# Kernel tuning notes

Hardware: AMD Instinct MI355X
Metric: run time of the kernel (lower is better)

Reference implementation:

```python
import jax, jax.numpy as jnp
import numpy as np

B, D, L = 64, 1024, 2048  # batch, init dim, source length; context feature dim = D//2


def setup_inputs() -> dict:
    key = jax.random.key(0)
    k1, k2, k3, k4 = jax.random.split(key, 4)
    inp = jax.random.normal(k1, (B, D), dtype=jnp.float32)
    context = jax.random.normal(k2, (B, L, D // 2), dtype=jnp.float32)
    # torch Linear weights: [out_features, in_features]
    W_in = jax.random.normal(k3, (D, D), dtype=jnp.float32) * (1.0 / np.sqrt(D))
    W_out = jax.random.normal(k4, (D, 2 * D), dtype=jnp.float32) * (1.0 / np.sqrt(2 * D))
    return {"input": inp, "context": context, "W_in": W_in, "W_out": W_out}


def reference(input, context, W_in, W_out):
    Bv, Dv = input.shape
    # linear_in(input).view(B, D//2, 2): two query vectors of size D//2 per batch
    targetT = (input @ W_in.T).reshape(Bv, Dv // 2, 2)           # [B, D/2, 2]
    attn = jnp.einsum('bld,bdk->bkl', context, targetT)          # [B, 2, L]
    attn = jax.nn.softmax(attn, axis=-1)                         # softmax over sourceL
    weighted = jnp.einsum('bkl,bld->bkd', attn, context)         # [B, 2, D/2]
    weightedContext = weighted.reshape(Bv, Dv)                   # [B, D]
    combined = jnp.concatenate([weightedContext, input], axis=1) # [B, 2D]
    contextOutput = jnp.tanh(combined @ W_out.T)                 # [B, D]
    return contextOutput, attn[:, 0, :], attn[:, 1, :]
```

## Files before the change

### kernel.cpp

```cpp
#include <hip/hip_runtime.h>
#include <cmath>

#define NB 64
#define ND 1024
#define DH 512
#define NL 2048
#define NCHUNK 16
#define RPB 128
#define RPW 32
#define REC 520
#define KS 32

typedef float f4 __attribute__((ext_vector_type(4)));
__device__ __forceinline__ f4 ntld(const float* p) {
  return __builtin_nontemporal_load((const f4*)p);
}

template <int KK>
__global__ __launch_bounds__(256, 4) void k_gemm(const float* __restrict__ A,
                                                 const float* __restrict__ W,
                                                 float* __restrict__ part) {
  constexpr int SLAB = KK / KS;
  __shared__ float As[64][36];
  const int t = threadIdx.x;
  const int lane = t & 63;
  const int wv = t >> 6;
  const int k0 = blockIdx.y * SLAB;
  const int j0 = __builtin_amdgcn_readfirstlane((int)(blockIdx.x * 32 + wv * 8));
  const float* Wb = W + (size_t)j0 * KK + k0;

  float acc[8];
#pragma unroll
  for (int j = 0; j < 8; j++) acc[j] = 0.f;

  const int srow = t >> 2, sko = (t & 3) * 8;
  const float* sbase = A + (size_t)srow * KK + k0 + sko;

  for (int kc = 0; kc < SLAB; kc += 32) {
    float4 v0 = *(const float4*)(sbase + kc);
    float4 v1 = *(const float4*)(sbase + kc + 4);
    __syncthreads();
    *(float4*)&As[srow][sko]     = v0;
    *(float4*)&As[srow][sko + 4] = v1;
    __syncthreads();
#pragma unroll
    for (int kk = 0; kk < 32; kk += 4) {
      float4 av = *(const float4*)&As[lane][kk];
      const float* wp = Wb + kc + kk;
#pragma unroll
      for (int j = 0; j < 8; j++) {
        float4 wq = *(const float4*)(wp + (size_t)j * KK);
        acc[j] = fmaf(av.x, wq.x, acc[j]);
        acc[j] = fmaf(av.y, wq.y, acc[j]);
        acc[j] = fmaf(av.z, wq.z, acc[j]);
        acc[j] = fmaf(av.w, wq.w, acc[j]);
      }
    }
  }
  float* p = part + ((size_t)blockIdx.y * 64 + lane) * ND + j0;
  *(float4*)(p)     = make_float4(acc[0], acc[1], acc[2], acc[3]);
  *(float4*)(p + 4) = make_float4(acc[4], acc[5], acc[6], acc[7]);
}

template <int ACT>
__global__ __launch_bounds__(64) void k_reduce(const float* __restrict__ part,
                                               float* __restrict__ out) {
  const int i = (blockIdx.x * 64 + threadIdx.x) * 4;
  float4 s = make_float4(0.f, 0.f, 0.f, 0.f);
#pragma unroll 8
  for (int ks = 0; ks < KS; ks++) {
    f4 v = ntld(part + (size_t)ks * (64 * ND) + i);
    s.x += v.x; s.y += v.y; s.z += v.z; s.w += v.w;
  }
  if (ACT) { s.x = tanhf(s.x); s.y = tanhf(s.y); s.z = tanhf(s.z); s.w = tanhf(s.w); }
  *(float4*)(out + i) = s;
}

__global__ __launch_bounds__(256, 4) void k2_attn(const float* __restrict__ ctx,
                                                  const float* __restrict__ tgt,
                                                  float* __restrict__ sc0,
                                                  float* __restrict__ sc1,
                                                  float* __restrict__ part) {
  const int chunk = blockIdx.x, b = blockIdx.y;
  const int wave = threadIdx.x >> 6, lane = threadIdx.x & 63;
  const float* crow = ctx + ((size_t)b * NL + chunk * RPB + wave * RPW) * DH + lane * 8;

  float t0[8], t1[8];
  {
    const float* tp = tgt + b * ND + lane * 16;
#pragma unroll
    for (int j = 0; j < 4; j++) {
      float4 v = *(const float4*)(tp + j * 4);
      t0[2 * j] = v.x; t1[2 * j] = v.y; t0[2 * j + 1] = v.z; t1[2 * j + 1] = v.w;
    }
  }

  float m0 = -INFINITY, l0 = 0.f, m1 = -INFINITY, l1 = 0.f;
  float a0[8], a1[8];
#pragma unroll
  for (int j = 0; j < 8; j++) { a0[j] = 0.f; a1[j] = 0.f; }
  float sv0 = 0.f, sv1 = 0.f;

  f4 cur[4], nxt[4];
  cur[0] = ntld(crow);
  cur[1] = ntld(crow + 4);
  cur[2] = ntld(crow + DH);
  cur[3] = ntld(crow + DH + 4);

#pragma unroll 2
  for (int ib = 0; ib < 16; ib++) {
    if (ib < 15) {
      const float* p = crow + (size_t)(2 * ib + 2) * DH;
      nxt[0] = ntld(p);
      nxt[1] = ntld(p + 4);
      nxt[2] = ntld(p + DH);
      nxt[3] = ntld(p + DH + 4);
    }
    const float* C = (const float*)cur;

    float s0[2], s1[2];
#pragma unroll
    for (int r = 0; r < 2; r++) {
      float x0 = 0.f, x1 = 0.f;
#pragma unroll
      for (int j = 0; j < 8; j++) { x0 += C[r * 8 + j] * t0[j]; x1 += C[r * 8 + j] * t1[j]; }
      s0[r] = x0; s1[r] = x1;
    }
#pragma unroll
    for (int off = 32; off; off >>= 1) {
      s0[0] += __shfl_xor(s0[0], off);
      s0[1] += __shfl_xor(s0[1], off);
      s1[0] += __shfl_xor(s1[0], off);
      s1[1] += __shfl_xor(s1[1], off);
    }
#pragma unroll
    for (int r = 0; r < 2; r++)
      if (lane == 2 * ib + r) { sv0 = s0[r]; sv1 = s1[r]; }

    {
      float mn = fmaxf(m0, fmaxf(s0[0], s0[1]));
      float al = __expf(m0 - mn);
      float p0 = __expf(s0[0] - mn), p1 = __expf(s0[1] - mn);
      l0 = l0 * al + p0 + p1;
      m0 = mn;
#pragma unroll
      for (int j = 0; j < 8; j++)
        a0[j] = a0[j] * al + p0 * C[j] + p1 * C[8 + j];
    }
    {
      float mn = fmaxf(m1, fmaxf(s1[0], s1[1]));
      float al = __expf(m1 - mn);
      float p0 = __expf(s1[0] - mn), p1 = __expf(s1[1] - mn);
      l1 = l1 * al + p0 + p1;
      m1 = mn;
#pragma unroll
      for (int j = 0; j < 8; j++)
        a1[j] = a1[j] * al + p0 * C[j] + p1 * C[8 + j];
    }
#pragma unroll
    for (int i = 0; i < 4; i++) cur[i] = nxt[i];
  }

  const int rowbase = b * NL + chunk * RPB + wave * RPW;
  if (lane < RPW) { sc0[rowbase + lane] = sv0; sc1[rowbase + lane] = sv1; }

  __shared__ float accS[4][1024];
  __shared__ float mlS[4][4];
  *(float4*)&accS[wave][lane * 8]           = make_float4(a0[0], a0[1], a0[2], a0[3]);
  *(float4*)&accS[wave][lane * 8 + 4]       = make_float4(a0[4], a0[5], a0[6], a0[7]);
  *(float4*)&accS[wave][512 + lane * 8]     = make_float4(a1[0], a1[1], a1[2], a1[3]);
  *(float4*)&accS[wave][512 + lane * 8 + 4] = make_float4(a1[4], a1[5], a1[6], a1[7]);
  if (lane == 0) { mlS[wave][0] = m0; mlS[wave][1] = l0; mlS[wave][2] = m1; mlS[wave][3] = l1; }
  __syncthreads();

  const int t = threadIdx.x;
  const int k = (t * 4) >> 9;
  const int d = (t * 4) & 511;
  float M = fmaxf(fmaxf(mlS[0][2 * k], mlS[1][2 * k]), fmaxf(mlS[2][2 * k], mlS[3][2 * k]));
  float Lk = 0.f;
  float v0 = 0.f, v1 = 0.f, v2 = 0.f, v3 = 0.f;
#pragma unroll
  for (int w = 0; w < 4; w++) {
    float e = __expf(mlS[w][2 * k] - M);
    Lk += mlS[w][2 * k + 1] * e;
    const float* ap = &accS[w][k * 512 + d];
    v0 += ap[0] * e; v1 += ap[1] * e; v2 += ap[2] * e; v3 += ap[3] * e;
  }
  float* rec = part + ((size_t)(b * NCHUNK + chunk) * 2 + k) * REC;
  if ((t & 127) == 0) { rec[0] = M; rec[1] = Lk; }
  *(float4*)&rec[4 + d] = make_float4(v0, v1, v2, v3);
}

__global__ __launch_bounds__(256) void k3_combine(const float* __restrict__ part,
                                                  const float* __restrict__ inp,
                                                  float* __restrict__ combined,
                                                  float* __restrict__ sc0,
                                                  float* __restrict__ sc1) {
  const int b = blockIdx.x >> 2, q = blockIdx.x & 3;
  const int t = threadIdx.x;
  __shared__ float MM[2], LL[2];
  __shared__ float eS[2][NCHUNK];
  if (t < 2) {
    const int k = t;
    float Mk = -INFINITY;
#pragma unroll
    for (int c = 0; c < NCHUNK; c++)
      Mk = fmaxf(Mk, part[((size_t)(b * NCHUNK + c) * 2 + k) * REC]);
    float Lk = 0.f;
#pragma unroll
    for (int c = 0; c < NCHUNK; c++) {
      const float* rec = part + ((size_t)(b * NCHUNK + c) * 2 + k) * REC;
      Lk += rec[1] * __expf(rec[0] - Mk);
    }
    MM[k] = Mk; LL[k] = Lk;
  }
  __syncthreads();
  if (t < 2 * NCHUNK) {
    const int k = t >> 4, c = t & 15;
    eS[k][c] = __expf(part[((size_t)(b * NCHUNK + c) * 2 + k) * REC] - MM[k]);
  }
  __syncthreads();

  const int k = t >> 7, d = q * 128 + (t & 127);
  float v = 0.f;
#pragma unroll
  for (int c = 0; c < NCHUNK; c++)
    v += part[((size_t)(b * NCHUNK + c) * 2 + k) * REC + 4 + d] * eS[k][c];
  combined[(size_t)b * 2048 + k * 512 + d] = v / LL[k];

  combined[(size_t)b * 2048 + 1024 + q * 256 + t] = inp[(size_t)b * ND + q * 256 + t];

  const float M0 = MM[0], i0 = 1.f / LL[0];
  const float M1 = MM[1], i1 = 1.f / LL[1];
  const int pos = b * NL + q * 512 + t * 2;
  float2 x0 = *(const float2*)(sc0 + pos);
  float2 x1 = *(const float2*)(sc1 + pos);
  x0.x = __expf(x0.x - M0) * i0; x0.y = __expf(x0.y - M0) * i0;
  x1.x = __expf(x1.x - M1) * i1; x1.y = __expf(x1.y - M1) * i1;
  *(float2*)(sc0 + pos) = x0;
  *(float2*)(sc1 + pos) = x1;
}

extern "C" void kernel_launch(void* const* d_in, const int* in_sizes, int n_in,
                              void* d_out, int out_size, void* d_ws, size_t ws_size,
                              hipStream_t stream) {
  const float* input   = (const float*)d_in[0];
  const float* context = (const float*)d_in[1];
  const float* W_in    = (const float*)d_in[2];
  const float* W_out   = (const float*)d_in[3];

  float* out   = (float*)d_out;
  float* attn0 = out + NB * ND;
  float* attn1 = attn0 + NB * NL;

  float* ws       = (float*)d_ws;
  float* target   = ws;
  float* combined = target + NB * ND;
  float* apart    = combined + NB * 2048;
  float* gpart    = apart + NB * NCHUNK * 2 * REC;

  k_gemm<ND><<<dim3(32, KS), dim3(256), 0, stream>>>(input, W_in, gpart);
  k_reduce<0><<<dim3(256), dim3(64), 0, stream>>>(gpart, target);
  k2_attn<<<dim3(NCHUNK, NB), dim3(256), 0, stream>>>(context, target, attn0, attn1, apart);
  k3_combine<<<dim3(4 * NB), dim3(256), 0, stream>>>(apart, input, combined, attn0, attn1);
  k_gemm<2 * ND><<<dim3(32, KS), dim3(256), 0, stream>>>(combined, W_out, gpart);
  k_reduce<1><<<dim3(256), dim3(64), 0, stream>>>(gpart, out);
}
```

Before: 391.9 us.

## Fuse combine and final reduce into producers via last-block atomic counters

Drops the separate combine and final reduce launches. The last attention block to finish for each batch row, and the last k-slab block for each output column tile of the second GEMM, now does the cross-block merge. Completion is detected with agent-scope atomic counters that are reset in the first reduce kernel. This removes two kernel launches and their gaps. In exchange the final merge runs on only a few blocks, which serialises that tail work, and the change adds threadfence and atomic overhead.

```diff
diff --git a/kernel.cpp b/kernel.cpp
--- a/kernel.cpp
+++ b/kernel.cpp
@@ -16,10 +16,12 @@
   return __builtin_nontemporal_load((const f4*)p);
 }
 
-template <int KK>
+template <int KK, int FUSE>
 __global__ __launch_bounds__(256, 4) void k_gemm(const float* __restrict__ A,
                                                  const float* __restrict__ W,
-                                                 float* __restrict__ part) {
+                                                 float* __restrict__ part,
+                                                 float* __restrict__ out,
+                                                 unsigned* __restrict__ cnt) {
   constexpr int SLAB = KK / KS;
   __shared__ float As[64][36];
   const int t = threadIdx.x;
@@ -60,11 +62,43 @@
   float* p = part + ((size_t)blockIdx.y * 64 + lane) * ND + j0;
   *(float4*)(p)     = make_float4(acc[0], acc[1], acc[2], acc[3]);
   *(float4*)(p + 4) = make_float4(acc[4], acc[5], acc[6], acc[7]);
-}
-
-template <int ACT>
-__global__ __launch_bounds__(64) void k_reduce(const float* __restrict__ part,
-                                               float* __restrict__ out) {
+
+  if constexpr (FUSE) {
+    __threadfence();
+    __shared__ unsigned lastS;
+    if (t == 0)
+      lastS = __hip_atomic_fetch_add(&cnt[blockIdx.x], 1u, __ATOMIC_ACQ_REL,
+                                     __HIP_MEMORY_SCOPE_AGENT);
+    __syncthreads();
+    if (lastS != KS - 1) return;
+    __threadfence();
+
+    const int jt = blockIdx.x * 32;
+    const int b = t >> 2, jj = (t & 3) * 8;
+    const float* gp = part + (size_t)b * ND + jt + jj;
+    float s[8];
+#pragma unroll
+    for (int x = 0; x < 8; x++) s[x] = 0.f;
+#pragma unroll 4
+    for (int ks = 0; ks < KS; ks++) {
+      f4 v0 = *(const f4*)(gp + (size_t)ks * (64 * ND));
+      f4 v1 = *(const f4*)(gp + (size_t)ks * (64 * ND) + 4);
+      s[0] += v0.x; s[1] += v0.y; s[2] += v0.z; s[3] += v0.w;
+      s[4] += v1.x; s[5] += v1.y; s[6] += v1.z; s[7] += v1.w;
+    }
+    float* op = out + (size_t)b * ND + jt + jj;
+    *(float4*)(op)     = make_float4(tanhf(s[0]), tanhf(s[1]), tanhf(s[2]), tanhf(s[3]));
+    *(float4*)(op + 4) = make_float4(tanhf(s[4]), tanhf(s[5]), tanhf(s[6]), tanhf(s[7]));
+  }
+}
+
+__global__ __launch_bounds__(64) void k_reduce0(const float* __restrict__ part,
+                                                float* __restrict__ outv,
+                                                unsigned* __restrict__ cnt) {
+  if (blockIdx.x == 0) {
+    cnt[threadIdx.x] = 0;
+    if (threadIdx.x < 32) cnt[64 + threadIdx.x] = 0;
+  }
   const int i = (blockIdx.x * 64 + threadIdx.x) * 4;
   float4 s = make_float4(0.f, 0.f, 0.f, 0.f);
 #pragma unroll 8
@@ -72,15 +106,17 @@
     f4 v = ntld(part + (size_t)ks * (64 * ND) + i);
     s.x += v.x; s.y += v.y; s.z += v.z; s.w += v.w;
   }
-  if (ACT) { s.x = tanhf(s.x); s.y = tanhf(s.y); s.z = tanhf(s.z); s.w = tanhf(s.w); }
-  *(float4*)(out + i) = s;
+  *(float4*)(outv + i) = s;
 }
 
 __global__ __launch_bounds__(256, 4) void k2_attn(const float* __restrict__ ctx,
                                                   const float* __restrict__ tgt,
                                                   float* __restrict__ sc0,
                                                   float* __restrict__ sc1,
-                                                  float* __restrict__ part) {
+                                                  float* __restrict__ part,
+                                                  float* __restrict__ combined,
+                                                  const float* __restrict__ inp,
+                                                  unsigned* __restrict__ cnt) {
   const int chunk = blockIdx.x, b = blockIdx.y;
   const int wave = threadIdx.x >> 6, lane = threadIdx.x & 63;
   const float* crow = ctx + ((size_t)b * NL + chunk * RPB + wave * RPW) * DH + lane * 8;
@@ -189,56 +225,72 @@
   float* rec = part + ((size_t)(b * NCHUNK + chunk) * 2 + k) * REC;
   if ((t & 127) == 0) { rec[0] = M; rec[1] = Lk; }
   *(float4*)&rec[4 + d] = make_float4(v0, v1, v2, v3);
-}
-
-__global__ __launch_bounds__(256) void k3_combine(const float* __restrict__ part,
-                                                  const float* __restrict__ inp,
-                                                  float* __restrict__ combined,
-                                                  float* __restrict__ sc0,
-                                                  float* __restrict__ sc1) {
-  const int b = blockIdx.x >> 2, q = blockIdx.x & 3;
-  const int t = threadIdx.x;
-  __shared__ float MM[2], LL[2];
-  __shared__ float eS[2][NCHUNK];
+
+  __threadfence();
+  __shared__ unsigned lastS;
+  if (t == 0)
+    lastS = __hip_atomic_fetch_add(&cnt[b], 1u, __ATOMIC_ACQ_REL,
+                                   __HIP_MEMORY_SCOPE_AGENT);
+  __syncthreads();
+  if (lastS != NCHUNK - 1) return;
+  __threadfence();
+
+  __shared__ float MM2[2], LL2[2];
+  __shared__ float eS2[2][NCHUNK];
   if (t < 2) {
-    const int k = t;
+    const int kq = t;
     float Mk = -INFINITY;
 #pragma unroll
     for (int c = 0; c < NCHUNK; c++)
-      Mk = fmaxf(Mk, part[((size_t)(b * NCHUNK + c) * 2 + k) * REC]);
-    float Lk = 0.f;
+      Mk = fmaxf(Mk, part[((size_t)(b * NCHUNK + c) * 2 + kq) * REC]);
+    float Lq = 0.f;
 #pragma unroll
     for (int c = 0; c < NCHUNK; c++) {
-      const float* rec = part + ((size_t)(b * NCHUNK + c) * 2 + k) * REC;
-      Lk += rec[1] * __expf(rec[0] - Mk);
-    }
-    MM[k] = Mk; LL[k] = Lk;
+      const float* rc = part + ((size_t)(b * NCHUNK + c) * 2 + kq) * REC;
+      Lq += rc[1] * __expf(rc[0] - Mk);
+    }
+    MM2[kq] = Mk; LL2[kq] = Lq;
   }
   __syncthreads();
   if (t < 2 * NCHUNK) {
-    const int k = t >> 4, c = t & 15;
-    eS[k][c] = __expf(part[((size_t)(b * NCHUNK + c) * 2 + k) * REC] - MM[k]);
+    const int kq = t >> 4, c = t & 15;
+    eS2[kq][c] = __expf(part[((size_t)(b * NCHUNK + c) * 2 + kq) * REC] - MM2[kq]);
   }
   __syncthreads();
 
-  const int k = t >> 7, d = q * 128 + (t & 127);
-  float v = 0.f;
-#pragma unroll
-  for (int c = 0; c < NCHUNK; c++)
-    v += part[((size_t)(b * NCHUNK + c) * 2 + k) * REC + 4 + d] * eS[k][c];
-  combined[(size_t)b * 2048 + k * 512 + d] = v / LL[k];
-
-  combined[(size_t)b * 2048 + 1024 + q * 256 + t] = inp[(size_t)b * ND + q * 256 + t];
-
-  const float M0 = MM[0], i0 = 1.f / LL[0];
-  const float M1 = MM[1], i1 = 1.f / LL[1];
-  const int pos = b * NL + q * 512 + t * 2;
-  float2 x0 = *(const float2*)(sc0 + pos);
-  float2 x1 = *(const float2*)(sc1 + pos);
-  x0.x = __expf(x0.x - M0) * i0; x0.y = __expf(x0.y - M0) * i0;
-  x1.x = __expf(x1.x - M1) * i1; x1.y = __expf(x1.y - M1) * i1;
-  *(float2*)(sc0 + pos) = x0;
-  *(float2*)(sc1 + pos) = x1;
+  {
+    const int kq = t >> 7, d0 = (t & 127) * 4;
+    float vx = 0.f, vy = 0.f, vz = 0.f, vw = 0.f;
+#pragma unroll
+    for (int c = 0; c < NCHUNK; c++) {
+      const f4 w = *(const f4*)(part + ((size_t)(b * NCHUNK + c) * 2 + kq) * REC + 4 + d0);
+      const float e = eS2[kq][c];
+      vx += w.x * e; vy += w.y * e; vz += w.z * e; vw += w.w * e;
+    }
+    const float invL = 1.f / LL2[kq];
+    *(float4*)(combined + (size_t)b * 2048 + kq * 512 + d0) =
+        make_float4(vx * invL, vy * invL, vz * invL, vw * invL);
+  }
+  *(float4*)(combined + (size_t)b * 2048 + 1024 + t * 4) =
+      *(const float4*)(inp + (size_t)b * ND + t * 4);
+
+  {
+    const float M0 = MM2[0], i0 = 1.f / LL2[0];
+    const float M1 = MM2[1], i1 = 1.f / LL2[1];
+    const int pos = b * NL + t * 8;
+    f4 xa = *(f4*)(sc0 + pos), xb = *(f4*)(sc0 + pos + 4);
+    xa.x = __expf(xa.x - M0) * i0; xa.y = __expf(xa.y - M0) * i0;
+    xa.z = __expf(xa.z - M0) * i0; xa.w = __expf(xa.w - M0) * i0;
+    xb.x = __expf(xb.x - M0) * i0; xb.y = __expf(xb.y - M0) * i0;
+    xb.z = __expf(xb.z - M0) * i0; xb.w = __expf(xb.w - M0) * i0;
+    *(f4*)(sc0 + pos) = xa; *(f4*)(sc0 + pos + 4) = xb;
+    f4 ya = *(f4*)(sc1 + pos), yb = *(f4*)(sc1 + pos + 4);
+    ya.x = __expf(ya.x - M1) * i1; ya.y = __expf(ya.y - M1) * i1;
+    ya.z = __expf(ya.z - M1) * i1; ya.w = __expf(ya.w - M1) * i1;
+    yb.x = __expf(yb.x - M1) * i1; yb.y = __expf(yb.y - M1) * i1;
+    yb.z = __expf(yb.z - M1) * i1; yb.w = __expf(yb.w - M1) * i1;
+    *(f4*)(sc1 + pos) = ya; *(f4*)(sc1 + pos + 4) = yb;
+  }
 }
 
 extern "C" void kernel_launch(void* const* d_in, const int* in_sizes, int n_in,
@@ -258,11 +310,12 @@
   float* combined = target + NB * ND;
   float* apart    = combined + NB * 2048;
   float* gpart    = apart + NB * NCHUNK * 2 * REC;
-
-  k_gemm<ND><<<dim3(32, KS), dim3(256), 0, stream>>>(input, W_in, gpart);
-  k_reduce<0><<<dim3(256), dim3(64), 0, stream>>>(gpart, target);
-  k2_attn<<<dim3(NCHUNK, NB), dim3(256), 0, stream>>>(context, target, attn0, attn1, apart);
-  k3_combine<<<dim3(4 * NB), dim3(256), 0, stream>>>(apart, input, combined, attn0, attn1);
-  k_gemm<2 * ND><<<dim3(32, KS), dim3(256), 0, stream>>>(combined, W_out, gpart);
-  k_reduce<1><<<dim3(256), dim3(64), 0, stream>>>(gpart, out);
-}
+  unsigned* cnts  = (unsigned*)(gpart + (size_t)KS * 64 * ND);
+
+  k_gemm<ND, 0><<<dim3(32, KS), dim3(256), 0, stream>>>(input, W_in, gpart, nullptr, nullptr);
+  k_reduce0<<<dim3(256), dim3(64), 0, stream>>>(gpart, target, cnts);
+  k2_attn<<<dim3(NCHUNK, NB), dim3(256), 0, stream>>>(context, target, attn0, attn1,
+                                                      apart, combined, input, cnts);
+  k_gemm<2 * ND, 1><<<dim3(32, KS), dim3(256), 0, stream>>>(combined, W_out, gpart,
+                                                            out, cnts + 64);
+}
```

New measurement: 823.9 us. 110% more time.
